# Kernel optimization log

Hardware: AMD Instinct MI355X
Metric: run time of the kernel (lower is better)

The kernel has to match this reference:

```python
import jax, jax.numpy as jnp
import numpy as np

N_EMBD = 1024  # C in forward; scale is C**-0.5 (full embed dim, per source)


def setup_inputs() -> dict:
    key = jax.random.key(0)
    k1, k2, k3, k4 = jax.random.split(key, 4)
    B, T, C, H = 4, 4096, N_EMBD, 64
    x = jax.random.normal(k1, (B, T, C), dtype=jnp.float32)
    # weights stored as [in, out] = [n_embd, head_size]
    Wq = jax.random.normal(k2, (C, H), dtype=jnp.float32) * (C ** -0.5)
    Wk = jax.random.normal(k3, (C, H), dtype=jnp.float32) * (C ** -0.5)
    Wv = jax.random.normal(k4, (C, H), dtype=jnp.float32) * (C ** -0.5)
    return {"x": x, "Wq": Wq, "Wk": Wk, "Wv": Wv}


def reference(x, Wq, Wk, Wv):
    # x: [B, T, C]; projections to head_size H
    C = x.shape[-1]
    q = jnp.einsum('btc,ch->bth', x, Wq)  # [B,T,H]
    k = jnp.einsum('btc,ch->bth', x, Wk)  # [B,T,H]
    v = jnp.einsum('btc,ch->bth', x, Wv)  # [B,T,H]
    # scores scaled by C**-0.5 (full embed dim, matching original module)
    wei = jnp.einsum('bth,bsh->bts', q, k) * (C ** -0.5)  # [B,T,T]
    wei = jax.nn.softmax(wei, axis=-1)  # dropout p=0 -> identity
    out = jnp.einsum('bts,bsh->bth', wei, v)  # [B,T,H]
    return out
```

## Files before the change

kernel.cpp:

```cpp
#include <hip/hip_runtime.h>
#include <hip/hip_bf16.h>


#define BB 4
#define TT 4096
#define CC 1024
#define HH 64

typedef __attribute__((ext_vector_type(8))) short bf16x8;
typedef __attribute__((ext_vector_type(4))) float f32x4;

#if __has_builtin(__builtin_amdgcn_exp2f)
#define EXP2(x) __builtin_amdgcn_exp2f(x)
#else
#define EXP2(x) exp2f(x)
#endif

__device__ __forceinline__ short f2bf(float f) {
  union { float f; unsigned u; } v; v.f = f;
  unsigned r = v.u + 0x7fffu + ((v.u >> 16) & 1u);
  return (short)(r >> 16);
}

__device__ __forceinline__ unsigned pk2bf(float lo, float hi) {
  __hip_bfloat162 p = __float22bfloat162_rn(make_float2(lo, hi));
  return *reinterpret_cast<unsigned*>(&p);
}

__device__ __forceinline__ void gload16(const short* g, short* l) {
  __builtin_amdgcn_global_load_lds(
      (const __attribute__((address_space(1))) void*)g,
      (__attribute__((address_space(3))) void*)l, 16, 0, 0);
}

#define WAITVM0() asm volatile("s_waitcnt vmcnt(0)" ::: "memory")

__global__ void wtf_kernel(const float* __restrict__ Wq, const float* __restrict__ Wk,
                           const float* __restrict__ Wv, short* __restrict__ WtF) {
  int idx = blockIdx.x * 256 + threadIdx.x;
  int lane = idx & 63, ks = (idx >> 6) & 31, nf = idx >> 11;
  int l15 = lane & 15, lg = lane >> 4;
  int n = nf * 16 + l15;
  const float* W = (n < HH) ? Wq : ((n < 2 * HH) ? Wk : Wv);
  float sc = (n < HH) ? (0.03125f * 1.44269504f) : 1.0f;
  int k0 = ks * 32 + lg * 8, h = n & (HH - 1);
  bf16x8 r;
#pragma unroll
  for (int j = 0; j < 8; ++j) r[j] = f2bf(W[(k0 + j) * HH + h] * sc);
  *(bf16x8*)(WtF + (size_t)idx * 8) = r;
}

__global__ void xc_kernel(const float* __restrict__ x, short* __restrict__ xF) {
  int idx = blockIdx.x * 256 + threadIdx.x;
  int lane = idx & 63, ks = (idx >> 6) & 31, rt = idx >> 11;
  int l15 = lane & 15, lg = lane >> 4;
  const float4* src = (const float4*)(x + (size_t)(rt * 16 + l15) * CC + ks * 32 + lg * 8);
  float4 a = src[0], b = src[1];
  uint4 w;
  w.x = pk2bf(a.x, a.y);  w.y = pk2bf(a.z, a.w);
  w.z = pk2bf(b.x, b.y);  w.w = pk2bf(b.z, b.w);
  *(uint4*)(xF + (size_t)idx * 8) = w;
}

__launch_bounds__(256, 4)
__global__ void projG_kernel(const short* __restrict__ xF, const short* __restrict__ WtF,
                             short* __restrict__ qo, short* __restrict__ kFo,
                             short* __restrict__ vFo) {
  __shared__ __align__(16) short xs[16384];
  int t = threadIdx.x;
  int row0 = blockIdx.x * 16;
  int wave = t >> 6, lane = t & 63;
  int l15 = lane & 15, lg = lane >> 4;

  {
    const short* gsrc = xF + (size_t)blockIdx.x * 16384 + ((size_t)wave * 512 + lane) * 8;
    short* ldst = xs + (size_t)wave * 4096;
#pragma unroll
    for (int k2 = 0; k2 < 8; ++k2)
      gload16(gsrc + k2 * 512, ldst + k2 * 512);
  }

  int nf0 = wave * 3;
  const short* wp = WtF + ((size_t)nf0 * 32 * 64 + (size_t)lane) * 8;

  f32x4 acc[3];
#pragma unroll
  for (int j = 0; j < 3; ++j) acc[j] = (f32x4){0.f, 0.f, 0.f, 0.f};

  WAITVM0();
  __syncthreads();

  bf16x8 wA[3], wB[3];
#pragma unroll
  for (int j = 0; j < 3; ++j) wA[j] = *(const bf16x8*)(wp + (size_t)j * 32 * 512);

#pragma unroll
  for (int ks = 0; ks < 32; ks += 2) {
#pragma unroll
    for (int j = 0; j < 3; ++j)
      wB[j] = *(const bf16x8*)(wp + ((size_t)j * 32 + ks + 1) * 512);
    bf16x8 a0 = *(const bf16x8*)(xs + ks * 512 + lane * 8);
#pragma unroll
    for (int j = 0; j < 3; ++j)
      acc[j] = __builtin_amdgcn_mfma_f32_16x16x32_bf16(a0, wA[j], acc[j], 0, 0, 0);
    if (ks + 2 < 32) {
#pragma unroll
      for (int j = 0; j < 3; ++j)
        wA[j] = *(const bf16x8*)(wp + ((size_t)j * 32 + ks + 2) * 512);
    }
    bf16x8 a1 = *(const bf16x8*)(xs + (ks + 1) * 512 + lane * 8);
#pragma unroll
    for (int j = 0; j < 3; ++j)
      acc[j] = __builtin_amdgcn_mfma_f32_16x16x32_bf16(a1, wB[j], acc[j], 0, 0, 0);
  }

  int b  = row0 >> 12;
  int kt = (row0 & 4095) >> 6;
  int cf = (row0 >> 4) & 3;
  short* ksl = xs;
  short* vsl = xs + 1152;

  __syncthreads();

#pragma unroll
  for (int j = 0; j < 3; ++j) {
    int nf = nf0 + j;
    int h = (nf & 3) * 16 + l15;
    if (nf < 4) {
#pragma unroll
      for (int reg = 0; reg < 4; ++reg)
        qo[(size_t)(row0 + lg * 4 + reg) * HH + h] = f2bf(acc[j][reg]);
    } else if (nf < 8) {
#pragma unroll
      for (int reg = 0; reg < 4; ++reg)
        ksl[(lg * 4 + reg) * 72 + h] = f2bf(acc[j][reg]);
    } else {
      uint2 w2;
      w2.x = pk2bf(acc[j][0], acc[j][1]);
      w2.y = pk2bf(acc[j][2], acc[j][3]);
      *(uint2*)(vsl + h * 24 + lg * 4) = w2;
    }
  }
  __syncthreads();

  size_t tileoff = ((size_t)b * 64 + kt) * 4096;
  if (t < 128) {
    int ks2 = t >> 6, ln = t & 63;
    int l15o = ln & 15, lgo = ln >> 4;
    bf16x8 r = *(const bf16x8*)(ksl + l15o * 72 + ks2 * 32 + lgo * 8);
    *(bf16x8*)(kFo + tileoff + (size_t)(cf * 2 + ks2) * 512 + ln * 8) = r;
  } else if (t < 256) {
    int t2 = t - 128;
    int hf = t2 >> 5, lgl = (t2 >> 4) & 1, l15o = t2 & 15;
    bf16x8 r = *(const bf16x8*)(vsl + (hf * 16 + l15o) * 24 + lgl * 8);
    int lnout = (2 * (cf & 1) + lgl) * 16 + l15o;
    *(bf16x8*)(vFo + tileoff + (size_t)(hf * 2 + (cf >> 1)) * 512 + lnout * 8) = r;
  }
}

__launch_bounds__(512, 4)
__global__ void attnW_kernel(const short* __restrict__ q, const short* __restrict__ kF,
                             const short* __restrict__ vF, float* __restrict__ out) {
  __shared__ __align__(16) short ps[8][2560];
  __shared__ __align__(16) float macc[32][68];
  __shared__ float lL[32];
  int wave = threadIdx.x >> 6, lane = threadIdx.x & 63;
  int l15 = lane & 15, lg = lane >> 4;
  int low3 = blockIdx.x & 7;
  int b  = low3 >> 1;
  int qt = ((blockIdx.x >> 3) << 1) | (low3 & 1);
  int brow0 = qt * 32;

  const short* qb = q + ((size_t)b * TT + brow0 + l15) * HH;
  bf16x8 qa[2][2];
#pragma unroll
  for (int g = 0; g < 2; ++g) {
    qa[g][0] = *(const bf16x8*)(qb + g * 16 * HH + lg * 8);
    qa[g][1] = *(const bf16x8*)(qb + g * 16 * HH + 32 + lg * 8);
  }

  bf16x8 ones;
#pragma unroll
  for (int j = 0; j < 8; ++j) ones[j] = (short)0x3F80;

  const short* kfb = kF + (size_t)b * 262144 + (size_t)lane * 8;
  const short* vfb = vF + (size_t)b * 262144 + (size_t)lane * 8;

  f32x4 acc[2][4], accl[2];
#pragma unroll
  for (int g = 0; g < 2; ++g) {
#pragma unroll
    for (int i = 0; i < 4; ++i) acc[g][i] = (f32x4){0.f, 0.f, 0.f, 0.f};
    accl[g] = (f32x4){0.f, 0.f, 0.f, 0.f};
  }

  char* psw = (char*)&ps[wave][0];
  int xorv = (l15 >> 3) << 4;
  int pwbase = l15 * 80;
  int pr = l15 * 80 + ((lg << 4) ^ xorv);

  for (int t = wave * 16; t < wave * 16 + 16; ++t) {
    const short* kp = kfb + (size_t)t * 2048;
    const short* vp = vfb + (size_t)(t >> 1) * 4096 + (size_t)(t & 1) * 512;
    bf16x8 kf[4], vf[4];
#pragma unroll
    for (int ld = 0; ld < 4; ++ld) kf[ld] = *(const bf16x8*)(kp + ld * 512);
#pragma unroll
    for (int hf = 0; hf < 4; ++hf) vf[hf] = *(const bf16x8*)(vp + hf * 1024);
#pragma unroll
    for (int g = 0; g < 2; ++g)
#pragma unroll
      for (int cf = 0; cf < 2; ++cf) {
        f32x4 t4 = (f32x4){0.f, 0.f, 0.f, 0.f};
        t4 = __builtin_amdgcn_mfma_f32_16x16x32_bf16(kf[cf * 2], qa[g][0], t4, 0, 0, 0);
        t4 = __builtin_amdgcn_mfma_f32_16x16x32_bf16(kf[cf * 2 + 1], qa[g][1], t4, 0, 0, 0);
        float p0 = EXP2(t4[0]), p1 = EXP2(t4[1]);
        float p2 = EXP2(t4[2]), p3 = EXP2(t4[3]);
        unsigned w01 = pk2bf(p0, p1);
        unsigned w23 = pk2bf(p2, p3);
        int cb = (cf << 5) + (lg << 3);
        *(unsigned*)(psw + g * 1280 + pwbase + ((cb) ^ xorv)) = w01;
        *(unsigned*)(psw + g * 1280 + pwbase + ((cb + 4) ^ xorv)) = w23;
      }
    bf16x8 pa0 = *(const bf16x8*)(psw + pr);
    bf16x8 pa1 = *(const bf16x8*)(psw + 1280 + pr);
    __builtin_amdgcn_s_setprio(1);
#pragma unroll
    for (int hf = 0; hf < 4; ++hf) {
      acc[0][hf] = __builtin_amdgcn_mfma_f32_16x16x32_bf16(pa0, vf[hf], acc[0][hf], 0, 0, 0);
      acc[1][hf] = __builtin_amdgcn_mfma_f32_16x16x32_bf16(pa1, vf[hf], acc[1][hf], 0, 0, 0);
    }
    accl[0] = __builtin_amdgcn_mfma_f32_16x16x32_bf16(pa0, ones, accl[0], 0, 0, 0);
    accl[1] = __builtin_amdgcn_mfma_f32_16x16x32_bf16(pa1, ones, accl[1], 0, 0, 0);
    __builtin_amdgcn_s_setprio(0);
  }

#pragma unroll
  for (int ph = 0; ph < 8; ++ph) {
    if (wave == ph) {
#pragma unroll
      for (int g = 0; g < 2; ++g)
#pragma unroll
        for (int reg = 0; reg < 4; ++reg) {
          int row = g * 16 + lg * 4 + reg;
          if (ph == 0) {
#pragma unroll
            for (int hf = 0; hf < 4; ++hf)
              macc[row][hf * 16 + l15] = acc[g][hf][reg];
            if (l15 == 0) lL[row] = accl[g][reg];
          } else {
#pragma unroll
            for (int hf = 0; hf < 4; ++hf)
              macc[row][hf * 16 + l15] += acc[g][hf][reg];
            if (l15 == 0) lL[row] += accl[g][reg];
          }
        }
    }
    __syncthreads();
  }

  {
    int tt = threadIdx.x;
    int r = tt >> 4, c0 = (tt & 15) * 4;
    float linv = 1.0f / lL[r];
    float4 o;
    o.x = macc[r][c0 + 0] * linv; o.y = macc[r][c0 + 1] * linv;
    o.z = macc[r][c0 + 2] * linv; o.w = macc[r][c0 + 3] * linv;
    *(float4*)(out + ((size_t)b * TT + brow0 + r) * HH + c0) = o;
  }
}

extern "C" void kernel_launch(void* const* d_in, const int* in_sizes, int n_in,
                              void* d_out, int out_size, void* d_ws, size_t ws_size,
                              hipStream_t stream) {
  const float* x  = (const float*)d_in[0];
  const float* Wq = (const float*)d_in[1];
  const float* Wk = (const float*)d_in[2];
  const float* Wv = (const float*)d_in[3];
  float* out = (float*)d_out;

  char* ws = (char*)d_ws;
  short* WtF = (short*)ws;
  short* q   = (short*)(ws + 0x080000);
  short* kF  = (short*)(ws + 0x280000);
  short* vF  = (short*)(ws + 0x480000);
  short* xF  = (short*)(ws + 0x680000);

  hipLaunchKernelGGL(wtf_kernel,   dim3(96),   dim3(256), 0, stream, Wq, Wk, Wv, WtF);
  hipLaunchKernelGGL(xc_kernel,    dim3(8192), dim3(256), 0, stream, x, xF);
  hipLaunchKernelGGL(projG_kernel, dim3(1024), dim3(256), 0, stream, xF, WtF, q, kF, vF);
  hipLaunchKernelGGL(attnW_kernel, dim3(512),  dim3(512), 0, stream, q, kF, vF, out);
}
```

Baseline: 73.82 us.

## Fuse fp32-to-bf16 conversion of x into projection kernel via direct LDS loads

Removes the separate xc_kernel pass that converted x to bf16 in a fragment layout and wrote it to workspace. The projection kernel now loads raw fp32 x tiles straight into LDS with an XOR swizzle and converts to bf16 when reading each MFMA operand. This eliminates one kernel launch and a full write plus re-read of the converted x buffer. In exchange LDS per block doubles and launch bounds drop to 2 blocks per CU, and conversion instructions are added inside the inner loop.

```diff
diff --git a/kernel.cpp b/kernel.cpp
--- a/kernel.cpp
+++ b/kernel.cpp
@@ -27,7 +27,7 @@
   return *reinterpret_cast<unsigned*>(&p);
 }
 
-__device__ __forceinline__ void gload16(const short* g, short* l) {
+__device__ __forceinline__ void gload16(const void* g, short* l) {
   __builtin_amdgcn_global_load_lds(
       (const __attribute__((address_space(1))) void*)g,
       (__attribute__((address_space(3))) void*)l, 16, 0, 0);
@@ -50,34 +50,28 @@
   *(bf16x8*)(WtF + (size_t)idx * 8) = r;
 }
 
-__global__ void xc_kernel(const float* __restrict__ x, short* __restrict__ xF) {
-  int idx = blockIdx.x * 256 + threadIdx.x;
-  int lane = idx & 63, ks = (idx >> 6) & 31, rt = idx >> 11;
-  int l15 = lane & 15, lg = lane >> 4;
-  const float4* src = (const float4*)(x + (size_t)(rt * 16 + l15) * CC + ks * 32 + lg * 8);
-  float4 a = src[0], b = src[1];
-  uint4 w;
-  w.x = pk2bf(a.x, a.y);  w.y = pk2bf(a.z, a.w);
-  w.z = pk2bf(b.x, b.y);  w.w = pk2bf(b.z, b.w);
-  *(uint4*)(xF + (size_t)idx * 8) = w;
-}
-
-__launch_bounds__(256, 4)
-__global__ void projG_kernel(const short* __restrict__ xF, const short* __restrict__ WtF,
+__launch_bounds__(256, 2)
+__global__ void projX_kernel(const float* __restrict__ x, const short* __restrict__ WtF,
                              short* __restrict__ qo, short* __restrict__ kFo,
                              short* __restrict__ vFo) {
-  __shared__ __align__(16) short xs[16384];
+  __shared__ __align__(16) short xs[32768];
   int t = threadIdx.x;
   int row0 = blockIdx.x * 16;
   int wave = t >> 6, lane = t & 63;
   int l15 = lane & 15, lg = lane >> 4;
 
   {
-    const short* gsrc = xF + (size_t)blockIdx.x * 16384 + ((size_t)wave * 512 + lane) * 8;
-    short* ldst = xs + (size_t)wave * 4096;
-#pragma unroll
-    for (int k2 = 0; k2 < 8; ++k2)
-      gload16(gsrc + k2 * 512, ldst + k2 * 512);
+    const float* xb = x + (size_t)row0 * CC;
+    int lp = lane ^ (lane >> 3);
+#pragma unroll
+    for (int k2 = 0; k2 < 16; ++k2) {
+      int ks = wave * 8 + (k2 >> 1);
+      int ln = (k2 & 1) * 32 + (lp >> 1);
+      int h  = lp & 1;
+      const float* src = xb + (size_t)(ln & 15) * CC + ks * 32 + (ln >> 4) * 8 + h * 4;
+      short* dst = xs + ((size_t)wave * 1024 + (size_t)k2 * 64) * 8;
+      gload16(src, dst);
+    }
   }
 
   int nf0 = wave * 3;
@@ -90,6 +84,20 @@
   WAITVM0();
   __syncthreads();
 
+  const char* xsb = (const char*)xs;
+  int m = (lane >> 2) & 7;
+  int roA = ((lane * 2) ^ m) * 16;
+  int roB = ((lane * 2 + 1) ^ m) * 16;
+
+#define LDA(KS, AV)                                                  \
+  {                                                                  \
+    float4 fa_ = *(const float4*)(xsb + (KS) * 2048 + roA);          \
+    float4 fb_ = *(const float4*)(xsb + (KS) * 2048 + roB);          \
+    unsigned* au_ = (unsigned*)&(AV);                                \
+    au_[0] = pk2bf(fa_.x, fa_.y); au_[1] = pk2bf(fa_.z, fa_.w);      \
+    au_[2] = pk2bf(fb_.x, fb_.y); au_[3] = pk2bf(fb_.z, fb_.w);      \
+  }
+
   bf16x8 wA[3], wB[3];
 #pragma unroll
   for (int j = 0; j < 3; ++j) wA[j] = *(const bf16x8*)(wp + (size_t)j * 32 * 512);
@@ -99,7 +107,8 @@
 #pragma unroll
     for (int j = 0; j < 3; ++j)
       wB[j] = *(const bf16x8*)(wp + ((size_t)j * 32 + ks + 1) * 512);
-    bf16x8 a0 = *(const bf16x8*)(xs + ks * 512 + lane * 8);
+    bf16x8 a0;
+    LDA(ks, a0)
 #pragma unroll
     for (int j = 0; j < 3; ++j)
       acc[j] = __builtin_amdgcn_mfma_f32_16x16x32_bf16(a0, wA[j], acc[j], 0, 0, 0);
@@ -108,11 +117,13 @@
       for (int j = 0; j < 3; ++j)
         wA[j] = *(const bf16x8*)(wp + ((size_t)j * 32 + ks + 2) * 512);
     }
-    bf16x8 a1 = *(const bf16x8*)(xs + (ks + 1) * 512 + lane * 8);
+    bf16x8 a1;
+    LDA(ks + 1, a1)
 #pragma unroll
     for (int j = 0; j < 3; ++j)
       acc[j] = __builtin_amdgcn_mfma_f32_16x16x32_bf16(a1, wB[j], acc[j], 0, 0, 0);
   }
+#undef LDA
 
   int b  = row0 >> 12;
   int kt = (row0 & 4095) >> 6;
@@ -284,10 +295,8 @@
   short* q   = (short*)(ws + 0x080000);
   short* kF  = (short*)(ws + 0x280000);
   short* vF  = (short*)(ws + 0x480000);
-  short* xF  = (short*)(ws + 0x680000);
 
   hipLaunchKernelGGL(wtf_kernel,   dim3(96),   dim3(256), 0, stream, Wq, Wk, Wv, WtF);
-  hipLaunchKernelGGL(xc_kernel,    dim3(8192), dim3(256), 0, stream, x, xF);
-  hipLaunchKernelGGL(projG_kernel, dim3(1024), dim3(256), 0, stream, xF, WtF, q, kF, vF);
+  hipLaunchKernelGGL(projX_kernel, dim3(1024), dim3(256), 0, stream, x, WtF, q, kF, vF);
   hipLaunchKernelGGL(attnW_kernel, dim3(512),  dim3(512), 0, stream, q, kF, vF, out);
 }
```

Result: faster. 65.16 us (-11.7%).
